# Kernel optimization log

Measured on AMD Instinct MI355X. Metric: run time of the kernel, lower is better.

The kernel has to match this reference:

```python
import jax, jax.numpy as jnp
import numpy as np

N_NODES = 100000


def setup_inputs() -> dict:
    key = jax.random.key(0)
    k1, k2, k3, k4, k5 = jax.random.split(key, 5)
    dim_in, dim_out = 128, 128
    x = jax.random.normal(k1, (N_NODES, dim_in), dtype=jnp.float32)
    edge_index = jax.random.randint(k2, (2, 1600000), 0, N_NODES, dtype=jnp.int64)
    # PyG SAGEConv params: lin_l (neighbor path, with bias), lin_r (root path, no bias)
    s = 1.0 / np.sqrt(dim_in)
    W_l = jax.random.uniform(k3, (dim_in, dim_out), jnp.float32, -s, s)
    b_l = jax.random.uniform(k4, (dim_out,), jnp.float32, -s, s)
    W_r = jax.random.uniform(k5, (dim_in, dim_out), jnp.float32, -s, s)
    return {"x": x, "edge_index": edge_index, "W_l": W_l, "b_l": b_l, "W_r": W_r}


def reference(x, edge_index, W_l, b_l, W_r):
    src, dst = edge_index[0], edge_index[1]
    # mean aggregation of source features onto target nodes
    gathered = x[src]                                   # [E, d_in]
    summed = jax.ops.segment_sum(gathered, dst, num_segments=N_NODES)
    ones = jnp.ones((edge_index.shape[1],), dtype=x.dtype)
    count = jax.ops.segment_sum(ones, dst, num_segments=N_NODES)
    agg = summed / jnp.maximum(count, 1.0)[:, None]     # [N, d_in]
    # out = lin_l(agg) + lin_r(x)
    return agg @ W_l + b_l + x @ W_r
```

## Files before the change

kernel.cpp:

```cpp
#include <hip/hip_runtime.h>

#define N_NODES 100000
#define DIM 128
#define NE 1600000
#define NTILES (N_NODES / 8)
#define GEMM_BLOCKS 2048
#define CHUNK 512
#define NCHUNK ((N_NODES + CHUNK - 1) / CHUNK)

#define WT_BLOCKS 128
#define NCOARSE 391
#define CPAD 16
#define CCAP 4608
#define CB_BLOCKS 512
#define EPA (NE / CB_BLOCKS)
#define BCAP 640
#define NFINE 3125
#define BK_CAP 1024

typedef unsigned short u16;
typedef __attribute__((ext_vector_type(8))) short bf16x8;
typedef __attribute__((ext_vector_type(4))) float f32x4;

__device__ __forceinline__ float bf2f(u16 h) {
  return __uint_as_float(((unsigned int)h) << 16);
}
__device__ __forceinline__ u16 f2bf(float f) {
  unsigned int u = __float_as_uint(f);
  unsigned int lsb = (u >> 16) & 1u;
  u += 0x7fffu + lsb;
  return (u16)(u >> 16);
}


__global__ __launch_bounds__(256) void prep_k(const float* __restrict__ x,
                                              const float* __restrict__ Wl,
                                              const float* __restrict__ Wr,
                                              u16* __restrict__ Ax,
                                              u16* __restrict__ Wt) {
  const int blk = blockIdx.x;
  if (blk < WT_BLOCKS) {
    int idx = blk * 256 + threadIdx.x;
    int n = idx >> 8;
    int k = idx & 255;
    float v = (k < 128) ? Wr[(size_t)k * DIM + n] : Wl[(size_t)(k - 128) * DIM + n];
    Wt[(size_t)n * 256 + k] = f2bf(v);
    return;
  }
  int t = (blk - WT_BLOCKS) * 256 + threadIdx.x;
  int row = t >> 5;
  int c = (t & 31) * 4;
  float4 v = *(const float4*)(x + (size_t)row * DIM + c);
  ushort4 o;
  o.x = f2bf(v.x); o.y = f2bf(v.y); o.z = f2bf(v.z); o.w = f2bf(v.w);
  *(ushort4*)(Ax + (size_t)row * DIM + c) = o;
}

__global__ __launch_bounds__(512) void coarse_bin_k(const int* __restrict__ ei,
                                                    int* __restrict__ curC,
                                                    int* __restrict__ binnedC) {
  __shared__ u16 keyS[EPA];
  __shared__ int recS[EPA];
  __shared__ u16 key2[EPA];
  __shared__ int rec2[EPA];
  __shared__ int hist[NCOARSE];
  __shared__ int off[NCOARSE];
  __shared__ int lcur[NCOARSE];
  __shared__ int gbase[NCOARSE];
  __shared__ int scanb[512];
  const int tid = threadIdx.x;
  const int e0 = blockIdx.x * EPA;

  for (int i = tid; i < NCOARSE; i += 512) hist[i] = 0;
  __syncthreads();
  for (int i = tid; i < EPA; i += 512) {
    int src = ei[e0 + i];
    int dst = ei[NE + e0 + i];
    keyS[i] = (u16)(dst >> 8);
    recS[i] = ((dst & 255) << 17) | src;
    atomicAdd(&hist[dst >> 8], 1);
  }
  __syncthreads();
  int v = (tid < NCOARSE) ? hist[tid] : 0;
  scanb[tid] = v;
  __syncthreads();
  for (int o = 1; o < 512; o <<= 1) {
    int add = (tid >= o) ? scanb[tid - o] : 0;
    __syncthreads();
    scanb[tid] += add;
    __syncthreads();
  }
  if (tid < NCOARSE) {
    int ex = scanb[tid] - v;
    off[tid] = ex;
    lcur[tid] = ex;
    gbase[tid] = v ? atomicAdd(&curC[tid * CPAD], v) : 0;
  }
  __syncthreads();
  for (int i = tid; i < EPA; i += 512) {
    int k = keyS[i];
    int p = atomicAdd(&lcur[k], 1);
    rec2[p] = recS[i];
    key2[p] = (u16)k;
  }
  __syncthreads();
  for (int i = tid; i < EPA; i += 512) {
    int k = key2[i];
    int gp = gbase[k] + (i - off[k]);
    if (gp < CCAP) binnedC[(size_t)k * CCAP + gp] = rec2[i];
  }
}

__global__ __launch_bounds__(256) void fine_bin_k(const int* __restrict__ curC,
                                                  const int* __restrict__ binnedC,
                                                  int* __restrict__ binned,
                                                  int* __restrict__ bcnt) {
  __shared__ int recS[CCAP];
  __shared__ int rec2[CCAP];
  __shared__ int hist[8];
  __shared__ int off[8];
  __shared__ int lcur[8];
  const int c = blockIdx.x;
  const int tid = threadIdx.x;
  int cnt = curC[c * CPAD];
  if (cnt > CCAP) cnt = CCAP;

  if (tid < 8) hist[tid] = 0;
  __syncthreads();
  for (int i = tid; i < cnt; i += 256) {
    int r = binnedC[(size_t)c * CCAP + i];
    recS[i] = r;
    atomicAdd(&hist[r >> 22], 1);
  }
  __syncthreads();
  if (tid < 8) {
    int vv = hist[tid];
    bcnt[c * 8 + tid] = vv > BCAP ? BCAP : vv;
  }
  if (tid == 0) {
    int a = 0;
#pragma unroll
    for (int k = 0; k < 8; ++k) { off[k] = a; lcur[k] = a; a += hist[k]; }
  }
  __syncthreads();
  for (int i = tid; i < cnt; i += 256) {
    int r = recS[i];
    int p = atomicAdd(&lcur[r >> 22], 1);
    rec2[p] = r;
  }
  __syncthreads();
  for (int i = tid; i < cnt; i += 256) {
    int r = rec2[i];
    int k = r >> 22;
    int sl = i - off[k];
    if (sl < BCAP)
      binned[(size_t)(c * 8 + k) * BCAP + sl] = r & 0x3FFFFF;
  }
}

__global__ __launch_bounds__(256) void aggB_k(const int* __restrict__ bcnt,
                                              const int* __restrict__ binned,
                                              const u16* __restrict__ Ax,
                                              u16* __restrict__ Ag) {
  __shared__ int recS[BK_CAP];
  __shared__ int srcS[BK_CAP];
  __shared__ int hist[32];
  __shared__ int off[32];
  __shared__ int curS[32];
  const int b = blockIdx.x;
  const size_t lo = (size_t)b * BCAP;
  int cnt = bcnt[b];
  if (cnt > BK_CAP) cnt = BK_CAP;

  if (threadIdx.x < 32) hist[threadIdx.x] = 0;
  __syncthreads();
  for (int i = threadIdx.x; i < cnt; i += 256) {
    int rec = __builtin_nontemporal_load(&binned[lo + i]);
    recS[i] = rec;
    atomicAdd(&hist[rec >> 17], 1);
  }
  __syncthreads();
  if (threadIdx.x < 32) off[threadIdx.x] = hist[threadIdx.x];
  __syncthreads();
  for (int st = 1; st < 32; st <<= 1) {
    int add = 0;
    if (threadIdx.x < 32 && threadIdx.x >= st) add = off[threadIdx.x - st];
    __syncthreads();
    if (threadIdx.x < 32) off[threadIdx.x] += add;
    __syncthreads();
  }
  if (threadIdx.x < 32) curS[threadIdx.x] = off[threadIdx.x] - hist[threadIdx.x];
  __syncthreads();
  for (int i = threadIdx.x; i < cnt; i += 256) {
    int rec = recS[i];
    int l = atomicAdd(&curS[rec >> 17], 1);
    srcS[l] = (rec & 0x1FFFF) << 7;
  }
  __syncthreads();

  const int wid = threadIdx.x >> 6;
  const int lane = threadIdx.x & 63;
  const int node0 = b * 32;
  for (int ln = wid; ln < 32; ln += 4) {
    int node = node0 + ln;
    int d = hist[ln];
    int e1 = off[ln];
    int j = e1 - d;
    float ax = 0.f, ay = 0.f;
    for (; j + 4 <= e1; j += 4) {
      int s0 = srcS[j], s1 = srcS[j + 1], s2 = srcS[j + 2], s3 = srcS[j + 3];
      unsigned u0 = *(const unsigned*)(Ax + (size_t)(s0 + lane * 2));
      unsigned u1 = *(const unsigned*)(Ax + (size_t)(s1 + lane * 2));
      unsigned u2 = *(const unsigned*)(Ax + (size_t)(s2 + lane * 2));
      unsigned u3 = *(const unsigned*)(Ax + (size_t)(s3 + lane * 2));
      ax += bf2f((u16)u0) + bf2f((u16)u1) + bf2f((u16)u2) + bf2f((u16)u3);
      ay += bf2f((u16)(u0 >> 16)) + bf2f((u16)(u1 >> 16)) +
            bf2f((u16)(u2 >> 16)) + bf2f((u16)(u3 >> 16));
    }
    for (; j < e1; ++j) {
      unsigned u0 = *(const unsigned*)(Ax + (size_t)(srcS[j] + lane * 2));
      ax += bf2f((u16)u0);
      ay += bf2f((u16)(u0 >> 16));
    }
    float scale = 1.0f / fmaxf((float)d, 1.0f);
    unsigned p = (unsigned)f2bf(ax * scale) | ((unsigned)f2bf(ay * scale) << 16);
    *(unsigned*)(Ag + (size_t)node * DIM + lane * 2) = p;
  }
}

__global__ __launch_bounds__(256) void gemm_mfma(const u16* __restrict__ Ax,
                                                 const u16* __restrict__ Ag,
                                                 const u16* __restrict__ Wt,
                                                 const float* __restrict__ bias,
                                                 float* __restrict__ out) {
  const int wave = threadIdx.x >> 6;
  const int lane = threadIdx.x & 63;
  const int m = lane & 15;
  const int q = lane >> 4;
  const int n0 = wave * 32;
  const int rt = blockIdx.x;

  bf16x8 Ac[8];
  const u16* apx = Ax + (size_t)(rt * 16 + m) * DIM + q * 8;
  const u16* apg = Ag + (size_t)(rt * 16 + m) * DIM + q * 8;
#pragma unroll
  for (int s = 0; s < 4; ++s) Ac[s] = *(const bf16x8*)(apx + s * 32);
#pragma unroll
  for (int s = 4; s < 8; ++s) Ac[s] = *(const bf16x8*)(apg + (s - 4) * 32);

  bf16x8 Bf[2][8];
#pragma unroll
  for (int t = 0; t < 2; ++t) {
    const u16* bp = Wt + (size_t)(n0 + t * 16 + m) * 256 + q * 8;
#pragma unroll
    for (int s = 0; s < 8; ++s) Bf[t][s] = *(const bf16x8*)(bp + s * 32);
  }
  const float b0 = bias[n0 + m];
  const float b1 = bias[n0 + 16 + m];

  f32x4 acc0 = {0.f, 0.f, 0.f, 0.f};
  f32x4 acc1 = {0.f, 0.f, 0.f, 0.f};
#pragma unroll
  for (int s = 0; s < 8; ++s) {
    acc0 = __builtin_amdgcn_mfma_f32_16x16x32_bf16(Ac[s], Bf[0][s], acc0, 0, 0, 0);
    acc1 = __builtin_amdgcn_mfma_f32_16x16x32_bf16(Ac[s], Bf[1][s], acc1, 0, 0, 0);
  }
  float* o = out + (size_t)(rt * 16 + q * 4) * DIM + n0 + m;
#pragma unroll
  for (int r = 0; r < 4; ++r) {
    o[(size_t)r * DIM] = acc0[r] + b0;
    o[(size_t)r * DIM + 16] = acc1[r] + b1;
  }
}

__global__ __launch_bounds__(256) void hist_k(const int* __restrict__ ei,
                                              int* __restrict__ deg) {
  int e = blockIdx.x * 256 + threadIdx.x;
  if (e < NE) atomicAdd(&deg[ei[NE + e]], 1);
}

__global__ __launch_bounds__(512) void scan_sum_k(const int* __restrict__ deg,
                                                  int* __restrict__ partials) {
  __shared__ int s[CHUNK];
  int i = blockIdx.x * CHUNK + threadIdx.x;
  s[threadIdx.x] = (i < N_NODES) ? deg[i] : 0;
  __syncthreads();
  for (int off = 256; off > 0; off >>= 1) {
    if (threadIdx.x < off) s[threadIdx.x] += s[threadIdx.x + off];
    __syncthreads();
  }
  if (threadIdx.x == 0) partials[blockIdx.x] = s[0];
}

__global__ __launch_bounds__(256) void scan_part_k(int* __restrict__ partials) {
  __shared__ int s[256];
  int t = threadIdx.x;
  int v = (t < NCHUNK) ? partials[t] : 0;
  s[t] = v;
  __syncthreads();
  for (int off = 1; off < 256; off <<= 1) {
    int add = (t >= off) ? s[t - off] : 0;
    __syncthreads();
    s[t] += add;
    __syncthreads();
  }
  if (t < NCHUNK) partials[t] = s[t] - v;
}

__global__ __launch_bounds__(512) void scan_out_k(const int* __restrict__ deg,
                                                  const int* __restrict__ partials,
                                                  int* __restrict__ offsets,
                                                  int* __restrict__ cursor) {
  __shared__ int s[CHUNK];
  int t = threadIdx.x;
  int i = blockIdx.x * CHUNK + t;
  int v = (i < N_NODES) ? deg[i] : 0;
  s[t] = v;
  __syncthreads();
  for (int off = 1; off < CHUNK; off <<= 1) {
    int add = (t >= off) ? s[t - off] : 0;
    __syncthreads();
    s[t] += add;
    __syncthreads();
  }
  if (i < N_NODES) {
    int excl = partials[blockIdx.x] + s[t] - v;
    offsets[i] = excl;
    cursor[i] = excl;
  }
  if (i == 0) offsets[N_NODES] = NE;
}

__global__ __launch_bounds__(256) void fill_k(const int* __restrict__ ei,
                                              int* __restrict__ cursor,
                                              int* __restrict__ csr) {
  int e = blockIdx.x * 256 + threadIdx.x;
  if (e < NE) {
    int dst = ei[NE + e];
    int pos = atomicAdd(&cursor[dst], 1);
    csr[pos] = ei[e];
  }
}

__global__ __launch_bounds__(256) void agg_f32_k(const int* __restrict__ offsets,
                                                 const int* __restrict__ csr,
                                                 const float* __restrict__ x,
                                                 float* __restrict__ agg) {
  int node = blockIdx.x * 4 + (threadIdx.x >> 6);
  int lane = threadIdx.x & 63;
  int beg = offsets[node], end = offsets[node + 1];
  float ax = 0.f, ay = 0.f;
  int i = beg;
  for (; i + 4 <= end; i += 4) {
    int s0 = csr[i], s1 = csr[i + 1], s2 = csr[i + 2], s3 = csr[i + 3];
    float2 v0 = *(const float2*)(x + (size_t)s0 * DIM + lane * 2);
    float2 v1 = *(const float2*)(x + (size_t)s1 * DIM + lane * 2);
    float2 v2 = *(const float2*)(x + (size_t)s2 * DIM + lane * 2);
    float2 v3 = *(const float2*)(x + (size_t)s3 * DIM + lane * 2);
    ax += v0.x + v1.x + v2.x + v3.x;
    ay += v0.y + v1.y + v2.y + v3.y;
  }
  for (; i < end; ++i) {
    float2 v0 = *(const float2*)(x + (size_t)csr[i] * DIM + lane * 2);
    ax += v0.x;
    ay += v0.y;
  }
  float scale = 1.0f / fmaxf((float)(end - beg), 1.0f);
  float2 r;
  r.x = ax * scale;
  r.y = ay * scale;
  *(float2*)(agg + (size_t)node * DIM + lane * 2) = r;
}

__global__ __launch_bounds__(256) void gemm_xw(const float* __restrict__ x,
                                               const float* __restrict__ W,
                                               const float* __restrict__ b,
                                               float* __restrict__ out) {
  __shared__ float Ws[DIM * DIM];
  for (int i = threadIdx.x; i < DIM * DIM; i += 256) Ws[i] = W[i];
  __syncthreads();
  const int c = threadIdx.x & 127;
  const int half = threadIdx.x >> 7;
  const float bias = b[c];
  for (int tile = blockIdx.x; tile < NTILES; tile += gridDim.x) {
    const int row0 = tile * 8 + half * 4;
    const float* r = x + (size_t)row0 * DIM;
    float a0 = 0.f, a1 = 0.f, a2 = 0.f, a3 = 0.f;
#pragma unroll 8
    for (int k4 = 0; k4 < 32; ++k4) {
      float4 p0 = *(const float4*)(r + 0 * DIM + k4 * 4);
      float4 p1 = *(const float4*)(r + 1 * DIM + k4 * 4);
      float4 p2 = *(const float4*)(r + 2 * DIM + k4 * 4);
      float4 p3 = *(const float4*)(r + 3 * DIM + k4 * 4);
      const float* wp = &Ws[k4 * 4 * DIM + c];
      float w0 = wp[0 * DIM], w1 = wp[1 * DIM], w2 = wp[2 * DIM], w3 = wp[3 * DIM];
      a0 += p0.x * w0 + p0.y * w1 + p0.z * w2 + p0.w * w3;
      a1 += p1.x * w0 + p1.y * w1 + p1.z * w2 + p1.w * w3;
      a2 += p2.x * w0 + p2.y * w1 + p2.z * w2 + p2.w * w3;
      a3 += p3.x * w0 + p3.y * w1 + p3.z * w2 + p3.w * w3;
    }
    out[(size_t)(row0 + 0) * DIM + c] = a0 + bias;
    out[(size_t)(row0 + 1) * DIM + c] = a1 + bias;
    out[(size_t)(row0 + 2) * DIM + c] = a2 + bias;
    out[(size_t)(row0 + 3) * DIM + c] = a3 + bias;
  }
}

__global__ __launch_bounds__(256) void gemm_aw(const float* __restrict__ agg,
                                               const float* __restrict__ W,
                                               float* __restrict__ out) {
  __shared__ float Ws[DIM * DIM];
  for (int i = threadIdx.x; i < DIM * DIM; i += 256) Ws[i] = W[i];
  __syncthreads();
  const int c = threadIdx.x & 127;
  const int half = threadIdx.x >> 7;
  for (int tile = blockIdx.x; tile < NTILES; tile += gridDim.x) {
    const int row0 = tile * 8 + half * 4;
    const float* r = agg + (size_t)row0 * DIM;
    float a0 = 0.f, a1 = 0.f, a2 = 0.f, a3 = 0.f;
#pragma unroll 8
    for (int k4 = 0; k4 < 32; ++k4) {
      float4 p0 = *(const float4*)(r + 0 * DIM + k4 * 4);
      float4 p1 = *(const float4*)(r + 1 * DIM + k4 * 4);
      float4 p2 = *(const float4*)(r + 2 * DIM + k4 * 4);
      float4 p3 = *(const float4*)(r + 3 * DIM + k4 * 4);
      const float* wp = &Ws[k4 * 4 * DIM + c];
      float w0 = wp[0 * DIM], w1 = wp[1 * DIM], w2 = wp[2 * DIM], w3 = wp[3 * DIM];
      a0 += p0.x * w0 + p0.y * w1 + p0.z * w2 + p0.w * w3;
      a1 += p1.x * w0 + p1.y * w1 + p1.z * w2 + p1.w * w3;
      a2 += p2.x * w0 + p2.y * w1 + p2.z * w2 + p2.w * w3;
      a3 += p3.x * w0 + p3.y * w1 + p3.z * w2 + p3.w * w3;
    }
    out[(size_t)(row0 + 0) * DIM + c] += a0;
    out[(size_t)(row0 + 1) * DIM + c] += a1;
    out[(size_t)(row0 + 2) * DIM + c] += a2;
    out[(size_t)(row0 + 3) * DIM + c] += a3;
  }
}

extern "C" void kernel_launch(void* const* d_in, const int* in_sizes, int n_in,
                              void* d_out, int out_size, void* d_ws, size_t ws_size,
                              hipStream_t stream) {
  const float* x  = (const float*)d_in[0];
  const int*   ei = (const int*)d_in[1];
  const float* Wl = (const float*)d_in[2];
  const float* bl = (const float*)d_in[3];
  const float* Wr = (const float*)d_in[4];
  float* out = (float*)d_out;

  u16* Ax       = (u16*)d_ws;
  u16* Ag       = Ax + (size_t)N_NODES * DIM;
  u16* Wt       = Ag + (size_t)N_NODES * DIM;
  int* curC     = (int*)(Wt + 128 * 256);
  int* bcnt     = curC + NCOARSE * CPAD;
  int* binnedC  = (int*)d_out;
  int* binned   = binnedC + (size_t)NCOARSE * CCAP;
  size_t needed = (size_t)N_NODES * DIM * 2 * 2 + 65536 +
                  (NCOARSE * CPAD + 3200) * 4;

  if (ws_size >= needed) {
    hipMemsetAsync(curC, 0, NCOARSE * CPAD * sizeof(int), stream);
    hipLaunchKernelGGL(prep_k, dim3(WT_BLOCKS + 12500), dim3(256), 0, stream,
                       x, Wl, Wr, Ax, Wt);
    hipLaunchKernelGGL(coarse_bin_k, dim3(CB_BLOCKS), dim3(512), 0, stream,
                       ei, curC, binnedC);
    hipLaunchKernelGGL(fine_bin_k, dim3(NCOARSE), dim3(256), 0, stream,
                       curC, binnedC, binned, bcnt);
    hipLaunchKernelGGL(aggB_k, dim3(NFINE), dim3(256), 0, stream,
                       bcnt, binned, Ax, Ag);
    hipLaunchKernelGGL(gemm_mfma, dim3(N_NODES / 16), dim3(256), 0, stream,
                       Ax, Ag, Wt, bl, out);
  } else {
    int* deg2      = (int*)d_ws;
    int* offsets2  = deg2 + N_NODES;
    int* partials2 = offsets2 + 100004;
    int* csr2      = partials2 + 256;
    float* agg     = (float*)(csr2 + NE);
    hipMemsetAsync(deg2, 0, (size_t)N_NODES * sizeof(int), stream);
    hipLaunchKernelGGL(hist_k, dim3((NE + 255) / 256), dim3(256), 0, stream, ei, deg2);
    hipLaunchKernelGGL(scan_sum_k, dim3(NCHUNK), dim3(CHUNK), 0, stream, deg2, partials2);
    hipLaunchKernelGGL(scan_part_k, dim3(1), dim3(256), 0, stream, partials2);
    hipLaunchKernelGGL(scan_out_k, dim3(NCHUNK), dim3(CHUNK), 0, stream,
                       deg2, partials2, offsets2, deg2);
    hipLaunchKernelGGL(fill_k, dim3((NE + 255) / 256), dim3(256), 0, stream,
                       ei, deg2, csr2);
    hipLaunchKernelGGL(agg_f32_k, dim3(N_NODES / 4), dim3(256), 0, stream,
                       offsets2, csr2, x, agg);
    hipLaunchKernelGGL(gemm_xw, dim3(GEMM_BLOCKS), dim3(256), 0, stream,
                       x, Wr, bl, out);
    hipLaunchKernelGGL(gemm_aw, dim3(GEMM_BLOCKS), dim3(256), 0, stream,
                       agg, Wl, out);
  }
}
```

Measured before the change: 272.0 us.

## Fuse neighbor aggregation with MFMA GEMM, keeping aggregated rows in LDS

Merges the aggregation kernel and the GEMM kernel. Each block now writes its 32 aggregated bf16 rows into shared memory and runs the MFMA projection on them directly. This removes the global write and re-read of the aggregated matrix and one kernel launch. The binned edge buffers move from the output buffer into the now-unused Ag workspace region, and output stores become nontemporal. In exchange the block uses more shared memory, and weight fragments are reloaded from global memory per block.

```diff
diff --git a/kernel.cpp b/kernel.cpp
--- a/kernel.cpp
+++ b/kernel.cpp
@@ -158,15 +158,18 @@
   }
 }
 
-__global__ __launch_bounds__(256) void aggB_k(const int* __restrict__ bcnt,
-                                              const int* __restrict__ binned,
-                                              const u16* __restrict__ Ax,
-                                              u16* __restrict__ Ag) {
+__global__ __launch_bounds__(256) void aggGemm_k(const int* __restrict__ bcnt,
+                                                 const int* __restrict__ binned,
+                                                 const u16* __restrict__ Ax,
+                                                 const u16* __restrict__ Wt,
+                                                 const float* __restrict__ bias,
+                                                 float* __restrict__ out) {
   __shared__ int recS[BK_CAP];
   __shared__ int srcS[BK_CAP];
+  __shared__ u16 aggS[32][136];
   __shared__ int hist[32];
   __shared__ int off[32];
-  __shared__ int curS[32];
+  __shared__ int cur[32];
   const int b = blockIdx.x;
   const size_t lo = (size_t)b * BCAP;
   int cnt = bcnt[b];
@@ -189,20 +192,18 @@
     if (threadIdx.x < 32) off[threadIdx.x] += add;
     __syncthreads();
   }
-  if (threadIdx.x < 32) curS[threadIdx.x] = off[threadIdx.x] - hist[threadIdx.x];
+  if (threadIdx.x < 32) cur[threadIdx.x] = off[threadIdx.x] - hist[threadIdx.x];
   __syncthreads();
   for (int i = threadIdx.x; i < cnt; i += 256) {
     int rec = recS[i];
-    int l = atomicAdd(&curS[rec >> 17], 1);
+    int l = atomicAdd(&cur[rec >> 17], 1);
     srcS[l] = (rec & 0x1FFFF) << 7;
   }
   __syncthreads();
 
-  const int wid = threadIdx.x >> 6;
+  const int wave = threadIdx.x >> 6;
   const int lane = threadIdx.x & 63;
-  const int node0 = b * 32;
-  for (int ln = wid; ln < 32; ln += 4) {
-    int node = node0 + ln;
+  for (int ln = wave; ln < 32; ln += 4) {
     int d = hist[ln];
     int e1 = off[ln];
     int j = e1 - d;
@@ -224,52 +225,59 @@
     }
     float scale = 1.0f / fmaxf((float)d, 1.0f);
     unsigned p = (unsigned)f2bf(ax * scale) | ((unsigned)f2bf(ay * scale) << 16);
-    *(unsigned*)(Ag + (size_t)node * DIM + lane * 2) = p;
-  }
-}
-
-__global__ __launch_bounds__(256) void gemm_mfma(const u16* __restrict__ Ax,
-                                                 const u16* __restrict__ Ag,
-                                                 const u16* __restrict__ Wt,
-                                                 const float* __restrict__ bias,
-                                                 float* __restrict__ out) {
-  const int wave = threadIdx.x >> 6;
-  const int lane = threadIdx.x & 63;
+    ((unsigned*)aggS)[ln * 68 + lane] = p;
+  }
+  __syncthreads();
+
   const int m = lane & 15;
   const int q = lane >> 4;
   const int n0 = wave * 32;
-  const int rt = blockIdx.x;
-
-  bf16x8 Ac[8];
-  const u16* apx = Ax + (size_t)(rt * 16 + m) * DIM + q * 8;
-  const u16* apg = Ag + (size_t)(rt * 16 + m) * DIM + q * 8;
-#pragma unroll
-  for (int s = 0; s < 4; ++s) Ac[s] = *(const bf16x8*)(apx + s * 32);
-#pragma unroll
-  for (int s = 4; s < 8; ++s) Ac[s] = *(const bf16x8*)(apg + (s - 4) * 32);
-
-  bf16x8 Bf[2][8];
-#pragma unroll
-  for (int t = 0; t < 2; ++t) {
-    const u16* bp = Wt + (size_t)(n0 + t * 16 + m) * 256 + q * 8;
-#pragma unroll
-    for (int s = 0; s < 8; ++s) Bf[t][s] = *(const bf16x8*)(bp + s * 32);
-  }
   const float b0 = bias[n0 + m];
   const float b1 = bias[n0 + 16 + m];
-
-  f32x4 acc0 = {0.f, 0.f, 0.f, 0.f};
-  f32x4 acc1 = {0.f, 0.f, 0.f, 0.f};
+  const u16* bp0 = Wt + (size_t)(n0 + m) * 256 + q * 8;
+  const u16* bp1 = Wt + (size_t)(n0 + 16 + m) * 256 + q * 8;
+
+#pragma clang loop unroll(disable)
+  for (int t = 0; t < 2; ++t) {
+    const int row = b * 32 + t * 16 + m;
+    f32x4 acc0 = {0.f, 0.f, 0.f, 0.f};
+    f32x4 acc1 = {0.f, 0.f, 0.f, 0.f};
+    {
+      const u16* apx = Ax + (size_t)row * DIM + q * 8;
+      bf16x8 A0 = *(const bf16x8*)(apx + 0 * 32);
+      bf16x8 A1 = *(const bf16x8*)(apx + 1 * 32);
+      bf16x8 A2 = *(const bf16x8*)(apx + 2 * 32);
+      bf16x8 A3 = *(const bf16x8*)(apx + 3 * 32);
+      acc0 = __builtin_amdgcn_mfma_f32_16x16x32_bf16(A0, *(const bf16x8*)(bp0 + 0 * 32), acc0, 0, 0, 0);
+      acc1 = __builtin_amdgcn_mfma_f32_16x16x32_bf16(A0, *(const bf16x8*)(bp1 + 0 * 32), acc1, 0, 0, 0);
+      acc0 = __builtin_amdgcn_mfma_f32_16x16x32_bf16(A1, *(const bf16x8*)(bp0 + 1 * 32), acc0, 0, 0, 0);
+      acc1 = __builtin_amdgcn_mfma_f32_16x16x32_bf16(A1, *(const bf16x8*)(bp1 + 1 * 32), acc1, 0, 0, 0);
+      acc0 = __builtin_amdgcn_mfma_f32_16x16x32_bf16(A2, *(const bf16x8*)(bp0 + 2 * 32), acc0, 0, 0, 0);
+      acc1 = __builtin_amdgcn_mfma_f32_16x16x32_bf16(A2, *(const bf16x8*)(bp1 + 2 * 32), acc1, 0, 0, 0);
+      acc0 = __builtin_amdgcn_mfma_f32_16x16x32_bf16(A3, *(const bf16x8*)(bp0 + 3 * 32), acc0, 0, 0, 0);
+      acc1 = __builtin_amdgcn_mfma_f32_16x16x32_bf16(A3, *(const bf16x8*)(bp1 + 3 * 32), acc1, 0, 0, 0);
+    }
+    {
+      const u16* apg = &aggS[t * 16 + m][q * 8];
+      bf16x8 A4 = *(const bf16x8*)(apg + 0 * 32);
+      bf16x8 A5 = *(const bf16x8*)(apg + 1 * 32);
+      bf16x8 A6 = *(const bf16x8*)(apg + 2 * 32);
+      bf16x8 A7 = *(const bf16x8*)(apg + 3 * 32);
+      acc0 = __builtin_amdgcn_mfma_f32_16x16x32_bf16(A4, *(const bf16x8*)(bp0 + 4 * 32), acc0, 0, 0, 0);
+      acc1 = __builtin_amdgcn_mfma_f32_16x16x32_bf16(A4, *(const bf16x8*)(bp1 + 4 * 32), acc1, 0, 0, 0);
+      acc0 = __builtin_amdgcn_mfma_f32_16x16x32_bf16(A5, *(const bf16x8*)(bp0 + 5 * 32), acc0, 0, 0, 0);
+      acc1 = __builtin_amdgcn_mfma_f32_16x16x32_bf16(A5, *(const bf16x8*)(bp1 + 5 * 32), acc1, 0, 0, 0);
+      acc0 = __builtin_amdgcn_mfma_f32_16x16x32_bf16(A6, *(const bf16x8*)(bp0 + 6 * 32), acc0, 0, 0, 0);
+      acc1 = __builtin_amdgcn_mfma_f32_16x16x32_bf16(A6, *(const bf16x8*)(bp1 + 6 * 32), acc1, 0, 0, 0);
+      acc0 = __builtin_amdgcn_mfma_f32_16x16x32_bf16(A7, *(const bf16x8*)(bp0 + 7 * 32), acc0, 0, 0, 0);
+      acc1 = __builtin_amdgcn_mfma_f32_16x16x32_bf16(A7, *(const bf16x8*)(bp1 + 7 * 32), acc1, 0, 0, 0);
+    }
+    float* o = out + (size_t)(b * 32 + t * 16 + q * 4) * DIM + n0 + m;
 #pragma unroll
-  for (int s = 0; s < 8; ++s) {
-    acc0 = __builtin_amdgcn_mfma_f32_16x16x32_bf16(Ac[s], Bf[0][s], acc0, 0, 0, 0);
-    acc1 = __builtin_amdgcn_mfma_f32_16x16x32_bf16(Ac[s], Bf[1][s], acc1, 0, 0, 0);
-  }
-  float* o = out + (size_t)(rt * 16 + q * 4) * DIM + n0 + m;
-#pragma unroll
-  for (int r = 0; r < 4; ++r) {
-    o[(size_t)r * DIM] = acc0[r] + b0;
-    o[(size_t)r * DIM + 16] = acc1[r] + b1;
+    for (int r = 0; r < 4; ++r) {
+      __builtin_nontemporal_store(acc0[r] + b0, &o[(size_t)r * DIM]);
+      __builtin_nontemporal_store(acc1[r] + b1, &o[(size_t)r * DIM + 16]);
+    }
   }
 }
 
@@ -450,11 +458,11 @@
 
   u16* Ax       = (u16*)d_ws;
   u16* Ag       = Ax + (size_t)N_NODES * DIM;
+  int* binnedC  = (int*)Ag;
+  int* binned   = binnedC + (size_t)NCOARSE * CCAP;
   u16* Wt       = Ag + (size_t)N_NODES * DIM;
   int* curC     = (int*)(Wt + 128 * 256);
   int* bcnt     = curC + NCOARSE * CPAD;
-  int* binnedC  = (int*)d_out;
-  int* binned   = binnedC + (size_t)NCOARSE * CCAP;
   size_t needed = (size_t)N_NODES * DIM * 2 * 2 + 65536 +
                   (NCOARSE * CPAD + 3200) * 4;
 
@@ -466,10 +474,8 @@
                        ei, curC, binnedC);
     hipLaunchKernelGGL(fine_bin_k, dim3(NCOARSE), dim3(256), 0, stream,
                        curC, binnedC, binned, bcnt);
-    hipLaunchKernelGGL(aggB_k, dim3(NFINE), dim3(256), 0, stream,
-                       bcnt, binned, Ax, Ag);
-    hipLaunchKernelGGL(gemm_mfma, dim3(N_NODES / 16), dim3(256), 0, stream,
-                       Ax, Ag, Wt, bl, out);
+    hipLaunchKernelGGL(aggGemm_k, dim3(NFINE), dim3(256), 0, stream,
+                       bcnt, binned, Ax, Wt, bl, out);
   } else {
     int* deg2      = (int*)d_ws;
     int* offsets2  = deg2 + N_NODES;
```

After: 240.7 us. -11.5%, faster.
